# Performance work log

Measured on AMD Instinct MI355X. Metric: run time of the kernel, lower is better.

## Reference

```python
import jax, jax.numpy as jnp
import numpy as np
from jax import lax

D_MODEL = 512
D_STATE = 32
D_CONV = 4
D_INNER = 2 * D_MODEL
DT_RANK = (D_MODEL + 15) // 16  # 32
B_SZ, L = 8, 1024
EPS = 1e-12


def _mamba_params(key, pfx):
    ks = jax.random.split(key, 6)
    s = 0.02
    p = {}
    p[pfx + '_in_w'] = jax.random.normal(ks[0], (2 * D_INNER, D_MODEL)) * s
    p[pfx + '_conv_w'] = jax.random.normal(ks[1], (D_INNER, D_CONV)) * s
    p[pfx + '_conv_b'] = jnp.zeros((D_INNER,))
    p[pfx + '_xproj_w'] = jax.random.normal(ks[2], (DT_RANK + 2 * D_STATE, D_INNER)) * s
    p[pfx + '_dt_w'] = jax.random.normal(ks[3], (D_INNER, DT_RANK)) * s
    p[pfx + '_dt_b'] = jax.random.uniform(ks[4], (D_INNER,), minval=-4.0, maxval=-2.0)
    p[pfx + '_A_log'] = jnp.log(jnp.broadcast_to(jnp.arange(1, D_STATE + 1, dtype=jnp.float32), (D_INNER, D_STATE)))
    p[pfx + '_D'] = jnp.ones((D_INNER,))
    p[pfx + '_out_w'] = jax.random.normal(ks[5], (D_MODEL, D_INNER)) * s
    return p


def setup_inputs() -> dict:
    key = jax.random.key(0)
    ks = jax.random.split(key, 10)
    inp = {
        'hidden_states': jax.random.normal(ks[0], (B_SZ, L, D_MODEL)),
        'lengths': jax.random.randint(ks[1], (B_SZ,), 1, L + 1, dtype=jnp.int32),
    }
    inp.update(_mamba_params(ks[2], 'f'))
    inp.update(_mamba_params(ks[3], 'b'))
    s = 0.02
    inp['proj_w'] = jax.random.normal(ks[4], (1, 2)) * 0.5 + 0.5
    inp['proj_b'] = jnp.zeros((1,))
    inp['ln_g'] = jnp.ones((D_MODEL,))
    inp['ln_b'] = jnp.zeros((D_MODEL,))
    inp['ffn_w1'] = jax.random.normal(ks[5], (4 * D_MODEL, D_MODEL)) * s
    inp['ffn_b1'] = jnp.zeros((4 * D_MODEL,))
    inp['ffn_w2'] = jax.random.normal(ks[6], (D_MODEL, 4 * D_MODEL)) * s
    inp['ffn_b2'] = jnp.zeros((D_MODEL,))
    inp['ffn_ln_g'] = jnp.ones((D_MODEL,))
    inp['ffn_ln_b'] = jnp.zeros((D_MODEL,))
    return inp


def _layernorm(x, g, b):
    mu = jnp.mean(x, -1, keepdims=True)
    var = jnp.mean(jnp.square(x - mu), -1, keepdims=True)
    return (x - mu) * lax.rsqrt(var + EPS) * g + b


def _selective_scan(delta, Bm, Cm, u, A, D):
    # delta,u: (B,L,Di); Bm,Cm: (B,L,N); A: (Di,N); D: (Di,)
    def step(h, inp):
        d_t, B_t, C_t, u_t = inp
        dA = jnp.exp(d_t[..., None] * A)                 # (B,Di,N)
        h = dA * h + (d_t * u_t)[..., None] * B_t[:, None, :]
        y = jnp.einsum('bdn,bn->bd', h, C_t)
        return h, y
    h0 = jnp.zeros((u.shape[0], A.shape[0], A.shape[1]), u.dtype)
    xs = (delta.transpose(1, 0, 2), Bm.transpose(1, 0, 2),
          Cm.transpose(1, 0, 2), u.transpose(1, 0, 2))
    _, ys = lax.scan(step, h0, xs)
    return ys.transpose(1, 0, 2) + u * D


def _mamba(x, in_w, conv_w, conv_b, xproj_w, dt_w, dt_b, A_log, Dp, out_w):
    xz = jnp.einsum('bld,ed->ble', x, in_w)              # (B,L,2Di)
    x_in, z = jnp.split(xz, 2, axis=-1)
    # causal depthwise conv1d
    xc = jnp.pad(x_in.transpose(0, 2, 1), ((0, 0), (0, 0), (D_CONV - 1, 0)))
    xc = lax.conv_general_dilated(xc, conv_w[:, None, :], (1,), 'VALID',
                                  dimension_numbers=('NCH', 'OIH', 'NCH'),
                                  feature_group_count=D_INNER)
    xc = jax.nn.silu(xc + conv_b[None, :, None]).transpose(0, 2, 1)  # (B,L,Di)
    x_dbl = jnp.einsum('bld,ed->ble', xc, xproj_w)
    dt, Bm, Cm = jnp.split(x_dbl, [DT_RANK, DT_RANK + D_STATE], axis=-1)
    delta = jax.nn.softplus(jnp.einsum('blr,dr->bld', dt, dt_w) + dt_b)
    A = -jnp.exp(A_log)
    y = _selective_scan(delta, Bm, Cm, xc, A, Dp)
    y = y * jax.nn.silu(z)
    return jnp.einsum('bld,ed->ble', y, out_w)


def reference(hidden_states, lengths,
              f_in_w, f_conv_w, f_conv_b, f_xproj_w, f_dt_w, f_dt_b, f_A_log, f_D, f_out_w,
              b_in_w, b_conv_w, b_conv_b, b_xproj_w, b_dt_w, b_dt_b, b_A_log, b_D, b_out_w,
              proj_w, proj_b, ln_g, ln_b,
              ffn_w1, ffn_b1, ffn_w2, ffn_b2, ffn_ln_g, ffn_ln_b):
    x = hidden_states
    hf = _mamba(x, f_in_w, f_conv_w, f_conv_b, f_xproj_w, f_dt_w, f_dt_b, f_A_log, f_D, f_out_w)
    hb = _mamba(jnp.flip(x, 1), b_in_w, b_conv_w, b_conv_b, b_xproj_w, b_dt_w, b_dt_b, b_A_log, b_D, b_out_w)
    hb = jnp.flip(hb, 1)
    # Linear(2,1) over stacked [hf,hb] on last axis
    out = hf * proj_w[0, 0] + hb * proj_w[0, 1] + proj_b[0]
    out1 = _layernorm(out + x, ln_g, ln_b)  # dropout = identity (eval)
    h = jax.nn.gelu(jnp.einsum('bld,ed->ble', out1, ffn_w1) + ffn_b1, approximate=False)
    h = jnp.einsum('ble,de->bld', h, ffn_w2) + ffn_b2
    return _layernorm(h + out1, ffn_ln_g, ffn_ln_b)
```

## Files before the change

kernel.cpp:

```cpp
#include <hip/hip_runtime.h>
#include <hip/hip_bf16.h>
#include <hip/hip_fp16.h>
#include <math.h>

typedef __hip_bfloat16 bf16;
typedef __attribute__((ext_vector_type(8))) short bfrag;
typedef __attribute__((ext_vector_type(4))) float ffrag;
typedef __attribute__((ext_vector_type(4))) float f4;
typedef __attribute__((ext_vector_type(4))) short sh4;

#define BSZ    8
#define LSEQ   1024
#define DMODEL 512
#define DINNER 1024
#define DSTATE 32
#define DTRANK 32
#define MROWS  (BSZ * LSEQ)

__device__ __forceinline__ float bf2f(bf16 v) { return __bfloat162float(v); }
__device__ __forceinline__ float s2f(short s) {
    union { unsigned u; float f; } c; c.u = ((unsigned)(unsigned short)s) << 16; return c.f;
}
__device__ __forceinline__ short f2s(float v) {
    union { bf16 b; short s; } u; u.b = __float2bfloat16(v); return u.s;
}
__device__ __forceinline__ void stC(float* p, size_t i, float v) { p[i] = v; }
__device__ __forceinline__ void stC(bf16* p, size_t i, float v) { p[i] = __float2bfloat16(v); }
__device__ __forceinline__ float fsigmoid(float x) {
    return __builtin_amdgcn_rcpf(1.f + __expf(-x));
}
__device__ __forceinline__ float fexp2(float x) { return __builtin_amdgcn_exp2f(x); }

__device__ __forceinline__ float dload(const void* p, size_t i, int f) {
    if (f == 1) return ((const float*)p)[i];
    if (f == 2) return __half2float(((const __half*)p)[i]);
    if (f == 3) return (float)((const double*)p)[i];
    return bf2f(((const bf16*)p)[i]);
}

enum { ACT_NONE = 0, ACT_SOFTPLUS = 1, ACT_GELU = 2 };

__global__ void resolve_kernel(const void* a8, const void* d9, const void* d22,
                               const void* s0, const void* s1, int* flags)
{
    if (threadIdx.x != 0 || blockIdx.x != 0) return;
    const int cand[4] = {1, 0, 2, 3};
    int fw = -1;
    for (int ci = 0; ci < 4 && fw < 0; ++ci) {
        int f = cand[ci];
        bool ok = true;
        for (int k = 0; k < 48 && ok; ++k) {
            float e = logf((float)((k & 31) + 1));
            float v = dload(a8, k, f);
            ok = (v == v) && fabsf(v - e) <= 0.02f * e + 0.02f;
        }
        for (int k = 0; k < 8 && ok; ++k)
            ok = fabsf(dload(d9, k, f) - 1.f) <= 0.01f &&
                 fabsf(dload(d22, k, f) - 1.f) <= 0.01f;
        if (ok) fw = f;
    }
    int fx = -1, xs = -1;
    for (int si = 0; si < 2 && fx < 0; ++si) {
        const void* p = (si == 0) ? s0 : s1;
        for (int ci = 0; ci < 4 && fx < 0; ++ci) {
            int f = cand[ci];
            bool ok = true;
            float s = 0.f, s2 = 0.f;
            for (int k = 0; k < 256 && ok; ++k) {
                float v = dload(p, k, f);
                ok = (v == v) && fabsf(v) < 16.f;
                s += v; s2 += v * v;
            }
            if (ok) {
                float mu = s * (1.f / 256.f);
                float var = s2 * (1.f / 256.f) - mu * mu;
                if (var > 0.25f && var < 4.f) { fx = f; xs = si; }
            }
        }
    }
    flags[0] = (fw < 0) ? 1 : fw;
    flags[1] = (fx < 0) ? 1 : fx;
    flags[2] = (xs < 0) ? 0 : xs;
    flags[3] = (fw == 1 && fx == 1) ? 1 : 0;
}

__global__ __launch_bounds__(256) void cvt_x_kernel(const void* x0, const void* x1,
                                                    bf16* __restrict__ dst,
                                                    const int* __restrict__ flags)
{
    const void* x = flags[2] ? x1 : x0;
    const int fx = flags[1];
    int i = blockIdx.x * 256 + threadIdx.x;
    if (fx == 1) {
        f4 v = ((const f4*)x)[i];
        sh4 o;
#pragma unroll
        for (int j = 0; j < 4; ++j) o[j] = f2s(v[j]);
        ((sh4*)dst)[i] = o;
    } else {
#pragma unroll
        for (int j = 0; j < 4; ++j)
            dst[(size_t)i * 4 + j] = __float2bfloat16(dload(x, (size_t)i * 4 + j, fx));
    }
}

__global__ __launch_bounds__(256) void cvt3_kernel(
    const float* __restrict__ s0, bf16* __restrict__ d0, int n0,
    const float* __restrict__ s1, bf16* __restrict__ d1, int n1,
    const float* __restrict__ s2, bf16* __restrict__ d2, int n2)
{
    int i = blockIdx.x * 256 + threadIdx.x;
    const float* s; bf16* d; int off;
    if (i < n0) { s = s0; d = d0; off = i; }
    else if (i < n0 + n1) { s = s1; d = d1; off = i - n0; }
    else if (i < n0 + n1 + n2) { s = s2; d = d2; off = i - n0 - n1; }
    else return;
    f4 v = ((const f4*)s)[off];
    sh4 o;
#pragma unroll
    for (int j = 0; j < 4; ++j) o[j] = f2s(v[j]);
    ((sh4*)d)[off] = o;
}

__global__ __launch_bounds__(256) void transpose_kernel(
    const bf16* __restrict__ src, bf16* __restrict__ dst, int R, int D)
{
    __shared__ short t[64][72];
    const int r0 = blockIdx.x * 64, d0 = blockIdx.y * 64;
    const int tr = threadIdx.x >> 3;
    const int tc = (threadIdx.x & 7) * 8;
#pragma unroll
    for (int h = 0; h < 2; ++h) {
        int d = tr + h * 32;
        bfrag v = *(const bfrag*)&src[(size_t)(d0 + d) * R + r0 + tc];
#pragma unroll
        for (int j = 0; j < 8; ++j) t[tc + j][d] = v[j];
    }
    __syncthreads();
#pragma unroll
    for (int h = 0; h < 2; ++h) {
        int r = tr + h * 32;
        bfrag v = *(const bfrag*)&t[r][tc];
        *(bfrag*)&dst[(size_t)(r0 + r) * D + d0 + tc] = v;
    }
}

__global__ __launch_bounds__(256) void transpose_f32_kernel(
    const float* __restrict__ src, float* __restrict__ dst, int R)
{
    __shared__ float t[64][68];
    const int m0 = blockIdx.x * 64;
    const int tr = threadIdx.x >> 2;
    const int tc = (threadIdx.x & 3) * 16;
#pragma unroll
    for (int j = 0; j < 4; ++j) {
        f4 v = *(const f4*)&src[(size_t)tr * R + m0 + tc + j * 4];
#pragma unroll
        for (int e = 0; e < 4; ++e) t[tc + j * 4 + e][tr] = v[e];
    }
    __syncthreads();
#pragma unroll
    for (int j = 0; j < 4; ++j) {
        f4 v = *(const f4*)&t[tr][tc + j * 4];
        *(f4*)&dst[(size_t)(m0 + tr) * 64 + tc + j * 4] = v;
    }
}

__device__ __forceinline__ void glds16(const bf16* g, short* l)
{
    __builtin_amdgcn_global_load_lds(
        (const __attribute__((address_space(1))) void*)g,
        (__attribute__((address_space(3))) void*)l,
        16, 0, 0);
}

template <int FLIPB, int ACT, typename CT>
__global__ __launch_bounds__(256) void bgemm_kernel(
    const bf16* __restrict__ A, int lda,
    const bf16* __restrict__ B, int ldb,
    const float* __restrict__ bias,
    CT* __restrict__ C, int ldc, int K)
{
    __shared__ __align__(16) short As[128 * 32];
    __shared__ __align__(16) short Bs[128 * 32];
    const int tid = threadIdx.x;
    const int bm = blockIdx.y * 128, bn = blockIdx.x * 128;
    const int lane = tid & 63, w = tid >> 6;

    const int srow = lane >> 2;
    const int skc  = (lane & 3) << 3;
    const int arow0 = bm + w * 32 + srow;
    int brow0 = bn + w * 32 + srow;
    int brow1 = brow0 + 16;
    if (FLIPB) {
        brow0 = (brow0 & ~(LSEQ - 1)) + (LSEQ - 1 - (brow0 & (LSEQ - 1)));
        brow1 = (brow1 & ~(LSEQ - 1)) + (LSEQ - 1 - (brow1 & (LSEQ - 1)));
    }
    const bf16* ga0 = A + (size_t)arow0 * lda + skc;
    const bf16* ga1 = ga0 + (size_t)16 * lda;
    const bf16* gb0 = B + (size_t)brow0 * ldb + skc;
    const bf16* gb1 = B + (size_t)brow1 * ldb + skc;
    short* la0 = &As[(w * 32) * 32];
    short* la1 = &As[(w * 32 + 16) * 32];
    short* lb0 = &Bs[(w * 32) * 32];
    short* lb1 = &Bs[(w * 32 + 16) * 32];

    const int wm = (w & 1) << 6, wn = (w >> 1) << 6;
    const int lm = lane & 15, quad = lane >> 4;

    ffrag acc[4][4];
#pragma unroll
    for (int i = 0; i < 4; ++i)
#pragma unroll
        for (int j = 0; j < 4; ++j)
#pragma unroll
            for (int e = 0; e < 4; ++e) acc[i][j][e] = 0.f;

    for (int k0 = 0; k0 < K; k0 += 32) {
        glds16(ga0 + k0, la0);
        glds16(ga1 + k0, la1);
        glds16(gb0 + k0, lb0);
        glds16(gb1 + k0, lb1);
        __syncthreads();
        bfrag af[4], bfv[4];
#pragma unroll
        for (int ti = 0; ti < 4; ++ti)
            af[ti] = *(const bfrag*)&As[(wm + ti * 16 + lm) * 32 + quad * 8];
#pragma unroll
        for (int tj = 0; tj < 4; ++tj)
            bfv[tj] = *(const bfrag*)&Bs[(wn + tj * 16 + lm) * 32 + quad * 8];
#pragma unroll
        for (int ti = 0; ti < 4; ++ti)
#pragma unroll
            for (int tj = 0; tj < 4; ++tj)
                acc[ti][tj] = __builtin_amdgcn_mfma_f32_16x16x32_bf16(
                    af[ti], bfv[tj], acc[ti][tj], 0, 0, 0);
        __syncthreads();
    }

#pragma unroll
    for (int tj = 0; tj < 4; ++tj) {
        int col = bn + wn + tj * 16 + lm;
        float bcv = bias ? bias[col] : 0.f;
#pragma unroll
        for (int ti = 0; ti < 4; ++ti) {
#pragma unroll
            for (int r2 = 0; r2 < 4; ++r2) {
                int rowg = bm + wm + ti * 16 + quad * 4 + r2;
                float v = acc[ti][tj][r2] + bcv;
                if (ACT == ACT_GELU) v = 0.5f * v * (1.f + erff(v * 0.70710678118654752f));
                stC(C, (size_t)rowg * ldc + col, v);
            }
        }
    }
}

template <int ACT, typename CT>
__global__ __launch_bounds__(256) void bgemm64_kernel(
    const bf16* __restrict__ A, int lda,
    const bf16* __restrict__ B, int ldb,
    const float* __restrict__ bias,
    CT* __restrict__ C, int ldc, int M, int K)
{
    __shared__ __align__(16) short As[128 * 64];
    __shared__ __align__(16) short Bs[64 * 64];
    const int tid = threadIdx.x;
    const int bm = blockIdx.y * 128, bn = blockIdx.x * 64;
    const int lane = tid & 63, w = tid >> 6;

    const int lr = lane >> 3;
    const int sc = ((lane & 7) ^ lr) << 3;

    const bf16* ga[4];
#pragma unroll
    for (int a = 0; a < 4; ++a) {
        int ar = bm + w * 32 + a * 8 + lr;
        if (ar >= M) ar = M - 1;
        ga[a] = A + (size_t)ar * lda + sc;
    }
    const bf16* gb[2];
#pragma unroll
    for (int a = 0; a < 2; ++a) {
        int br = bn + w * 16 + a * 8 + lr;
        gb[a] = B + (size_t)br * ldb + sc;
    }
    short* la = &As[(w * 32) * 64];
    short* lb = &Bs[(w * 16) * 64];

    const int wm = (w & 1) << 6, wn = (w >> 1) << 5;
    const int lm = lane & 15, quad = lane >> 4;

    ffrag acc[4][2];
#pragma unroll
    for (int i = 0; i < 4; ++i)
#pragma unroll
        for (int j = 0; j < 2; ++j)
#pragma unroll
            for (int e = 0; e < 4; ++e) acc[i][j][e] = 0.f;

    for (int k0 = 0; k0 < K; k0 += 64) {
#pragma unroll
        for (int a = 0; a < 4; ++a) glds16(ga[a] + k0, la + a * 8 * 64);
#pragma unroll
        for (int a = 0; a < 2; ++a) glds16(gb[a] + k0, lb + a * 8 * 64);
        __syncthreads();
        bfrag af[2][4], bfv[2][2];
#pragma unroll
        for (int kk = 0; kk < 2; ++kk) {
#pragma unroll
            for (int ti = 0; ti < 4; ++ti) {
                int row = wm + ti * 16 + lm;
                int c = kk * 4 + quad;
                af[kk][ti] = *(const bfrag*)&As[row * 64 + ((c ^ (row & 7)) << 3)];
            }
#pragma unroll
            for (int tj = 0; tj < 2; ++tj) {
                int row = wn + tj * 16 + lm;
                int c = kk * 4 + quad;
                bfv[kk][tj] = *(const bfrag*)&Bs[row * 64 + ((c ^ (row & 7)) << 3)];
            }
        }
#pragma unroll
        for (int kk = 0; kk < 2; ++kk)
#pragma unroll
            for (int ti = 0; ti < 4; ++ti)
#pragma unroll
                for (int tj = 0; tj < 2; ++tj)
                    acc[ti][tj] = __builtin_amdgcn_mfma_f32_16x16x32_bf16(
                        af[kk][ti], bfv[kk][tj], acc[ti][tj], 0, 0, 0);
        __syncthreads();
    }

#pragma unroll
    for (int tj = 0; tj < 2; ++tj) {
        int col = bn + wn + tj * 16 + lm;
        float bcv = bias ? bias[col] : 0.f;
#pragma unroll
        for (int ti = 0; ti < 4; ++ti) {
#pragma unroll
            for (int r2 = 0; r2 < 4; ++r2) {
                int rowg = bm + wm + ti * 16 + quad * 4 + r2;
                if (rowg < M) {
                    float v = acc[ti][tj][r2] + bcv;
                    if (ACT == ACT_GELU) v = 0.5f * v * (1.f + erff(v * 0.70710678118654752f));
                    stC(C, (size_t)rowg * ldc + col, v);
                }
            }
        }
    }
}

__global__ __launch_bounds__(256) void dt_kernel(
    const float* __restrict__ xdT,
    const float* __restrict__ dt_w,
    const float* __restrict__ dt_b,
    bf16* __restrict__ delta_T)
{
    const int m = blockIdx.x * 256 + threadIdx.x;
    const int d0 = blockIdx.y * 64;
    float v[32];
#pragma unroll
    for (int r = 0; r < 32; ++r) v[r] = xdT[(size_t)r * MROWS + m];
    for (int d = d0; d < d0 + 64; ++d) {
        float acc = dt_b[d];
#pragma unroll
        for (int r = 0; r < 32; ++r) acc = fmaf(dt_w[d * 32 + r], v[r], acc);
        acc = (acc > 20.f) ? acc : log1pf(__expf(acc));
        delta_T[(size_t)d * MROWS + m] = __float2bfloat16(acc);
    }
}

__global__ __launch_bounds__(256) void conv_silu_kernel(
    const bf16* __restrict__ xin_T,
    const void* __restrict__ cw,
    const void* __restrict__ cb,
    bf16* __restrict__ u_T,
    const int* __restrict__ flags)
{
    const int fw = flags[0];
    int blk = blockIdx.x;
    int chunk = blk & 3;
    int db = blk >> 2;
    int b = db & 7;
    int d = db >> 3;
    int l = chunk * 256 + threadIdx.x;
    size_t base = (size_t)d * MROWS + b * LSEQ;
    float w0 = dload(cw, d * 4 + 0, fw), w1 = dload(cw, d * 4 + 1, fw);
    float w2 = dload(cw, d * 4 + 2, fw), w3 = dload(cw, d * 4 + 3, fw);
    float acc = dload(cb, d, fw);
    if (l >= 3) acc += bf2f(xin_T[base + l - 3]) * w0;
    if (l >= 2) acc += bf2f(xin_T[base + l - 2]) * w1;
    if (l >= 1) acc += bf2f(xin_T[base + l - 1]) * w2;
    acc += bf2f(xin_T[base + l]) * w3;
    u_T[base + l] = __float2bfloat16(acc * fsigmoid(acc));
}

#define SCH 8
struct ScanBuf { float dl[SCH], uv[SCH], Bv[SCH], Cv[SCH]; float zsc, usc; };

__device__ __forceinline__ void scan_load(ScanBuf& s,
    const bf16* __restrict__ dT, const bf16* __restrict__ uT,
    const bf16* __restrict__ zT, const float* __restrict__ xm,
    size_t lb, size_t mb, int n)
{
    bfrag dv = *(const bfrag*)&dT[lb];
    bfrag uv = *(const bfrag*)&uT[lb];
#pragma unroll
    for (int j = 0; j < SCH; ++j) { s.dl[j] = s2f(dv[j]); s.uv[j] = s2f(uv[j]); }
    s.zsc = bf2f(zT[lb + (n & 7)]);
    s.usc = bf2f(uT[lb + (n & 7)]);
#pragma unroll
    for (int j = 0; j < SCH; ++j) {
        s.Bv[j] = xm[(mb + j) * 64 + n];
        s.Cv[j] = xm[(mb + j) * 64 + 32 + n];
    }
}

__device__ __forceinline__ void scan_compute(const ScanBuf& s, float& h,
    float Ad2, float Dd, bf16* __restrict__ yT, size_t lb,
    bool b0, bool b1, bool b2, bool wr)
{
    float p[SCH];
#pragma unroll
    for (int j = 0; j < SCH; ++j) {
        float dlv = s.dl[j];
        h = fexp2(dlv * Ad2) * h + dlv * s.uv[j] * s.Bv[j];
        p[j] = h * s.Cv[j];
    }
    float q[4];
#pragma unroll
    for (int jj = 0; jj < 4; ++jj) {
        float keep = b0 ? p[2 * jj + 1] : p[2 * jj];
        float send = b0 ? p[2 * jj] : p[2 * jj + 1];
        q[jj] = keep + __shfl_xor(send, 1);
    }
    float r0 = (b1 ? q[1] : q[0]) + __shfl_xor(b1 ? q[0] : q[1], 2);
    float r1 = (b1 ? q[3] : q[2]) + __shfl_xor(b1 ? q[2] : q[3], 2);
    float t = (b2 ? r1 : r0) + __shfl_xor(b2 ? r0 : r1, 4);
    t += __shfl_xor(t, 8);
    t += __shfl_xor(t, 16);
    if (wr) {
        float y = t + s.usc * Dd;
        float g = s.zsc;
        y *= g * fsigmoid(g);
        yT[lb + (threadIdx.x & 7)] = __float2bfloat16(y);
    }
}

__global__ __launch_bounds__(256) void scan_kernel(
    const bf16* __restrict__ delta_T,
    bf16* __restrict__ u_T,
    const bf16* __restrict__ z_T,
    const float* __restrict__ xdbl_m,
    const void* __restrict__ A_log,
    const void* __restrict__ Dp,
    const int* __restrict__ flags)
{
    const int fw = flags[0];
    const int tid = threadIdx.x;
    const int n = tid & 31;
    const int dloc = tid >> 5;
    const int gd = blockIdx.x * 8 + dloc;
    const int b = gd >> 10;
    const int d = gd & (DINNER - 1);
    const bool b0 = n & 1, b1 = n & 2, b2 = n & 4;
    const bool wr = (n < 8);

    const float Ad2 = -__expf(dload(A_log, d * DSTATE + n, fw)) * 1.44269504088896341f;
    const float Dd = dload(Dp, d, fw);
    const size_t lbase = (size_t)d * MROWS + b * LSEQ;
    const size_t mbase = (size_t)b * LSEQ;
    float h = 0.f;

    ScanBuf bufA, bufB;
    scan_load(bufA, delta_T, u_T, z_T, xdbl_m, lbase, mbase, n);
    for (int c0 = 0; c0 < LSEQ / SCH; c0 += 2) {
        scan_load(bufB, delta_T, u_T, z_T, xdbl_m,
                  lbase + (size_t)(c0 + 1) * SCH, mbase + (size_t)(c0 + 1) * SCH, n);
        scan_compute(bufA, h, Ad2, Dd, u_T, lbase + (size_t)c0 * SCH, b0, b1, b2, wr);
        if (c0 + 2 < LSEQ / SCH)
            scan_load(bufA, delta_T, u_T, z_T, xdbl_m,
                      lbase + (size_t)(c0 + 2) * SCH, mbase + (size_t)(c0 + 2) * SCH, n);
        scan_compute(bufB, h, Ad2, Dd, u_T, lbase + (size_t)(c0 + 1) * SCH, b0, b1, b2, wr);
    }
}

__global__ __launch_bounds__(256) void combine_ln_kernel(
    const bf16* __restrict__ hf, const bf16* __restrict__ hb,
    const void* __restrict__ x0, const void* __restrict__ x1,
    const void* __restrict__ pw, const void* __restrict__ pb,
    const void* __restrict__ g, const void* __restrict__ be,
    bf16* __restrict__ out1,
    const int* __restrict__ flags)
{
    const int fw = flags[0];
    const int fx = flags[1];
    const void* x = flags[2] ? x1 : x0;
    int row = blockIdx.x;
    int b = row >> 10, l = row & (LSEQ - 1);
    int rrow = (b << 10) + (LSEQ - 1 - l);
    float pw0 = dload(pw, 0, fw), pw1 = dload(pw, 1, fw), pbv = dload(pb, 0, fw);
    __shared__ float red[2][4];
    float v[2], s = 0.f, s2 = 0.f;
#pragma unroll
    for (int i = 0; i < 2; ++i) {
        int c = threadIdx.x + i * 256;
        float val = bf2f(hf[(size_t)row * DMODEL + c]) * pw0
                  + bf2f(hb[(size_t)rrow * DMODEL + c]) * pw1
                  + pbv + dload(x, (size_t)row * DMODEL + c, fx);
        v[i] = val; s += val; s2 += val * val;
    }
    for (int m = 1; m < 64; m <<= 1) { s += __shfl_xor(s, m); s2 += __shfl_xor(s2, m); }
    int w = threadIdx.x >> 6;
    if ((threadIdx.x & 63) == 0) { red[0][w] = s; red[1][w] = s2; }
    __syncthreads();
    s = red[0][0] + red[0][1] + red[0][2] + red[0][3];
    s2 = red[1][0] + red[1][1] + red[1][2] + red[1][3];
    float mu = s * (1.f / DMODEL);
    float var = s2 * (1.f / DMODEL) - mu * mu;
    float r = rsqrtf(fmaxf(var, 0.f) + 1e-12f);
#pragma unroll
    for (int i = 0; i < 2; ++i) {
        int c = threadIdx.x + i * 256;
        float val = (v[i] - mu) * r * dload(g, c, fw) + dload(be, c, fw);
        out1[(size_t)row * DMODEL + c] = __float2bfloat16(val);
    }
}

__global__ __launch_bounds__(256) void final_ln_kernel(
    const float* __restrict__ out2, const bf16* __restrict__ out1,
    const void* __restrict__ g, const void* __restrict__ be,
    float* __restrict__ out,
    const int* __restrict__ flags)
{
    const int fw = flags[0];
    const int valid = flags[3];
    int row = blockIdx.x;
    __shared__ float red[2][4];
    float v[2], s = 0.f, s2 = 0.f;
#pragma unroll
    for (int i = 0; i < 2; ++i) {
        int c = threadIdx.x + i * 256;
        float val = out2[(size_t)row * DMODEL + c] + bf2f(out1[(size_t)row * DMODEL + c]);
        v[i] = val; s += val; s2 += val * val;
    }
    for (int m = 1; m < 64; m <<= 1) { s += __shfl_xor(s, m); s2 += __shfl_xor(s2, m); }
    int w = threadIdx.x >> 6;
    if ((threadIdx.x & 63) == 0) { red[0][w] = s; red[1][w] = s2; }
    __syncthreads();
    s = red[0][0] + red[0][1] + red[0][2] + red[0][3];
    s2 = red[1][0] + red[1][1] + red[1][2] + red[1][3];
    float mu = s * (1.f / DMODEL);
    float var = s2 * (1.f / DMODEL) - mu * mu;
    float r = rsqrtf(fmaxf(var, 0.f) + 1e-12f);
#pragma unroll
    for (int i = 0; i < 2; ++i) {
        int c = threadIdx.x + i * 256;
        float val = (v[i] - mu) * r * dload(g, c, fw) + dload(be, c, fw);
        out[(size_t)row * DMODEL + c] = valid ? val : 0.f;
    }
}

extern "C" void kernel_launch(void* const* d_in, const int* in_sizes, int n_in,
                              void* d_out, int out_size, void* d_ws, size_t ws_size,
                              hipStream_t stream)
{
    const void* x0 = d_in[0];
    const void* x1 = d_in[1];
    const void* proj_w   = d_in[20];
    const void* proj_b   = d_in[21];
    const void* ln_g     = d_in[22];
    const void* ln_b     = d_in[23];
    const float* ffn_w1  = (const float*)d_in[24];
    const float* ffn_b1  = (const float*)d_in[25];
    const float* ffn_w2  = (const float*)d_in[26];
    const float* ffn_b2  = (const float*)d_in[27];
    const void* ffn_ln_g = d_in[28];
    const void* ffn_ln_b = d_in[29];

    char* wsb = (char*)d_ws;
    char* ob  = (char*)d_out;
    bf16*  xin_T   = (bf16*)(wsb + 0);
    bf16*  z_T     = (bf16*)(wsb + (16u << 20));
    bf16*  uy_T    = (bf16*)(wsb + (32u << 20));
    bf16*  u_rm    = (bf16*)(wsb + 0);
    bf16*  delta_T = (bf16*)(wsb + 0);
    bf16*  y_rm    = (bf16*)(wsb + 0);
    float* xdT     = (float*)(wsb + (48u << 20));
    bf16*  in_w_bf = (bf16*)(wsb + (51u << 20));
    float* xdbl_m  = (float*)(wsb + (51u << 20));
    bf16*  xp_w_bf = (bf16*)(wsb + (53u << 20));
    bf16*  o_w_bf  = (bf16*)(wsb + (54u << 20));
    bf16*  hf      = (bf16*)d_out;
    bf16*  hb      = (bf16*)d_out + (size_t)MROWS * DMODEL;
    bf16*  xbf     = (bf16*)(ob + (8u << 20));
    bf16*  w1bf    = (bf16*)(ob + 0);
    bf16*  w2bf    = (bf16*)(ob + (2u << 20));
    bf16*  out1    = (bf16*)(wsb + 0);
    bf16*  ffn_h   = (bf16*)(wsb + (8u << 20));
    float* out2    = (float*)(wsb + (40u << 20));
    int*   flags   = (int*)(wsb + (56u << 20));

    dim3 blk(256);

    resolve_kernel<<<dim3(1), dim3(64), 0, stream>>>(
        d_in[8], d_in[9], d_in[22], x0, x1, flags);
    cvt_x_kernel<<<dim3(4096), blk, 0, stream>>>(x0, x1, xbf, flags);

    for (int dir = 0; dir < 2; ++dir) {
        int pb0 = 2 + dir * 9;
        const float* in_w    = (const float*)d_in[pb0 + 0];
        const void*  conv_w  = d_in[pb0 + 1];
        const void*  conv_b  = d_in[pb0 + 2];
        const float* xproj_w = (const float*)d_in[pb0 + 3];
        const float* dt_w    = (const float*)d_in[pb0 + 4];
        const float* dt_b    = (const float*)d_in[pb0 + 5];
        const void*  A_log   = d_in[pb0 + 6];
        const void*  Dp      = d_in[pb0 + 7];
        const float* out_w   = (const float*)d_in[pb0 + 8];
        bf16* hout = (dir == 0) ? hf : hb;

        cvt3_kernel<<<dim3(1632), blk, 0, stream>>>(
            in_w, in_w_bf, (2048 * 512) / 4,
            xproj_w, xp_w_bf, (96 * 1024) / 4,
            out_w, o_w_bf, (512 * 1024) / 4);

        if (dir == 0)
            bgemm_kernel<0, ACT_NONE, bf16><<<dim3(64, 16), blk, 0, stream>>>(
                in_w_bf, DMODEL, xbf, DMODEL, nullptr, xin_T, MROWS, DMODEL);
        else
            bgemm_kernel<1, ACT_NONE, bf16><<<dim3(64, 16), blk, 0, stream>>>(
                in_w_bf, DMODEL, xbf, DMODEL, nullptr, xin_T, MROWS, DMODEL);

        conv_silu_kernel<<<dim3(DINNER * BSZ * 4), blk, 0, stream>>>(
            xin_T, conv_w, conv_b, uy_T, flags);
        transpose_kernel<<<dim3(128, 16), blk, 0, stream>>>(uy_T, u_rm, MROWS, DINNER);
        bgemm64_kernel<ACT_NONE, float><<<dim3(128, 1), blk, 0, stream>>>(
            xp_w_bf, DINNER, u_rm, DINNER, nullptr, xdT, MROWS, 96, DINNER);
        transpose_f32_kernel<<<dim3(128), blk, 0, stream>>>(
            xdT + (size_t)32 * MROWS, xdbl_m, MROWS);
        dt_kernel<<<dim3(32, 16), blk, 0, stream>>>(xdT, dt_w, dt_b, delta_T);
        scan_kernel<<<dim3((BSZ * DINNER) / 8), blk, 0, stream>>>(
            delta_T, uy_T, z_T, xdbl_m, A_log, Dp, flags);
        transpose_kernel<<<dim3(128, 16), blk, 0, stream>>>(uy_T, y_rm, MROWS, DINNER);
        bgemm64_kernel<ACT_NONE, bf16><<<dim3(8, 64), blk, 0, stream>>>(
            y_rm, DINNER, o_w_bf, DINNER, nullptr, hout, DMODEL, MROWS, DINNER);
    }

    combine_ln_kernel<<<dim3(MROWS), blk, 0, stream>>>(
        hf, hb, x0, x1, proj_w, proj_b, ln_g, ln_b, out1, flags);
    cvt3_kernel<<<dim3(2048), blk, 0, stream>>>(
        ffn_w1, w1bf, (2048 * 512) / 4,
        ffn_w2, w2bf, (512 * 2048) / 4,
        nullptr, nullptr, 0);
    bgemm_kernel<0, ACT_GELU, bf16><<<dim3(16, 64), blk, 0, stream>>>(
        out1, DMODEL, w1bf, DMODEL, ffn_b1, ffn_h, 2048, DMODEL);
    bgemm64_kernel<ACT_NONE, float><<<dim3(8, 64), blk, 0, stream>>>(
        ffn_h, 2048, w2bf, 2048, ffn_b2, out2, DMODEL, MROWS, 2048);
    final_ln_kernel<<<dim3(MROWS), blk, 0, stream>>>(
        out2, out1, ffn_ln_g, ffn_ln_b, (float*)d_out, flags);
}
```

Before: 925.8 us.

## Double-buffer LDS tiles in bf16 GEMMs and parallelize dtype-resolve kernel across a wavefront

Both GEMM kernels now keep two LDS buffers and issue the global-to-LDS loads for the next K tile before computing on the current one, so a single barrier per iteration replaces the load-then-sync pattern. The intent is to overlap memory latency with MFMA work. Shared memory use doubles, which can lower occupancy. The single-thread dtype detection kernel is also spread across a wavefront, using ballots and shuffle reductions to cut its serial latency.

New measurement: 869.3 us. -6.1%, faster.

```diff
diff --git a/kernel.cpp b/kernel.cpp
--- a/kernel.cpp
+++ b/kernel.cpp
@@ -43,21 +43,23 @@
 __global__ void resolve_kernel(const void* a8, const void* d9, const void* d22,
                                const void* s0, const void* s1, int* flags)
 {
-    if (threadIdx.x != 0 || blockIdx.x != 0) return;
+    if (blockIdx.x != 0) return;
+    const int lane = threadIdx.x;
     const int cand[4] = {1, 0, 2, 3};
     int fw = -1;
     for (int ci = 0; ci < 4 && fw < 0; ++ci) {
         int f = cand[ci];
         bool ok = true;
-        for (int k = 0; k < 48 && ok; ++k) {
-            float e = logf((float)((k & 31) + 1));
-            float v = dload(a8, k, f);
+        if (lane < 48) {
+            float e = logf((float)((lane & 31) + 1));
+            float v = dload(a8, lane, f);
             ok = (v == v) && fabsf(v - e) <= 0.02f * e + 0.02f;
-        }
-        for (int k = 0; k < 8 && ok; ++k)
+        } else if (lane < 56) {
+            int k = lane - 48;
             ok = fabsf(dload(d9, k, f) - 1.f) <= 0.01f &&
                  fabsf(dload(d22, k, f) - 1.f) <= 0.01f;
-        if (ok) fw = f;
+        }
+        if (__all(ok)) fw = f;
     }
     int fx = -1, xs = -1;
     for (int si = 0; si < 2 && fx < 0; ++si) {
@@ -66,22 +68,28 @@
             int f = cand[ci];
             bool ok = true;
             float s = 0.f, s2 = 0.f;
-            for (int k = 0; k < 256 && ok; ++k) {
+            for (int k = lane; k < 256; k += 64) {
                 float v = dload(p, k, f);
-                ok = (v == v) && fabsf(v) < 16.f;
+                ok = ok && (v == v) && fabsf(v) < 16.f;
                 s += v; s2 += v * v;
             }
-            if (ok) {
+            int allok = __all(ok);
+            for (int m = 1; m < 64; m <<= 1) {
+                s += __shfl_xor(s, m); s2 += __shfl_xor(s2, m);
+            }
+            if (allok) {
                 float mu = s * (1.f / 256.f);
                 float var = s2 * (1.f / 256.f) - mu * mu;
                 if (var > 0.25f && var < 4.f) { fx = f; xs = si; }
             }
         }
     }
-    flags[0] = (fw < 0) ? 1 : fw;
-    flags[1] = (fx < 0) ? 1 : fx;
-    flags[2] = (xs < 0) ? 0 : xs;
-    flags[3] = (fw == 1 && fx == 1) ? 1 : 0;
+    if (lane == 0) {
+        flags[0] = (fw < 0) ? 1 : fw;
+        flags[1] = (fx < 0) ? 1 : fx;
+        flags[2] = (xs < 0) ? 0 : xs;
+        flags[3] = (fw == 1 && fx == 1) ? 1 : 0;
+    }
 }
 
 __global__ __launch_bounds__(256) void cvt_x_kernel(const void* x0, const void* x1,
@@ -181,8 +189,8 @@
     const float* __restrict__ bias,
     CT* __restrict__ C, int ldc, int K)
 {
-    __shared__ __align__(16) short As[128 * 32];
-    __shared__ __align__(16) short Bs[128 * 32];
+    __shared__ __align__(16) short As[2][128 * 32];
+    __shared__ __align__(16) short Bs[2][128 * 32];
     const int tid = threadIdx.x;
     const int bm = blockIdx.y * 128, bn = blockIdx.x * 128;
     const int lane = tid & 63, w = tid >> 6;
@@ -200,10 +208,7 @@
     const bf16* ga1 = ga0 + (size_t)16 * lda;
     const bf16* gb0 = B + (size_t)brow0 * ldb + skc;
     const bf16* gb1 = B + (size_t)brow1 * ldb + skc;
-    short* la0 = &As[(w * 32) * 32];
-    short* la1 = &As[(w * 32 + 16) * 32];
-    short* lb0 = &Bs[(w * 32) * 32];
-    short* lb1 = &Bs[(w * 32 + 16) * 32];
+    const int lA0 = (w * 32) * 32, lA1 = (w * 32 + 16) * 32;
 
     const int wm = (w & 1) << 6, wn = (w >> 1) << 6;
     const int lm = lane & 15, quad = lane >> 4;
@@ -216,19 +221,27 @@
 #pragma unroll
             for (int e = 0; e < 4; ++e) acc[i][j][e] = 0.f;
 
+    glds16(ga0, &As[0][lA0]);
+    glds16(ga1, &As[0][lA1]);
+    glds16(gb0, &Bs[0][lA0]);
+    glds16(gb1, &Bs[0][lA1]);
+    __syncthreads();
+
+    int cur = 0;
     for (int k0 = 0; k0 < K; k0 += 32) {
-        glds16(ga0 + k0, la0);
-        glds16(ga1 + k0, la1);
-        glds16(gb0 + k0, lb0);
-        glds16(gb1 + k0, lb1);
-        __syncthreads();
+        if (k0 + 32 < K) {
+            glds16(ga0 + k0 + 32, &As[cur ^ 1][lA0]);
+            glds16(ga1 + k0 + 32, &As[cur ^ 1][lA1]);
+            glds16(gb0 + k0 + 32, &Bs[cur ^ 1][lA0]);
+            glds16(gb1 + k0 + 32, &Bs[cur ^ 1][lA1]);
+        }
         bfrag af[4], bfv[4];
 #pragma unroll
         for (int ti = 0; ti < 4; ++ti)
-            af[ti] = *(const bfrag*)&As[(wm + ti * 16 + lm) * 32 + quad * 8];
+            af[ti] = *(const bfrag*)&As[cur][(wm + ti * 16 + lm) * 32 + quad * 8];
 #pragma unroll
         for (int tj = 0; tj < 4; ++tj)
-            bfv[tj] = *(const bfrag*)&Bs[(wn + tj * 16 + lm) * 32 + quad * 8];
+            bfv[tj] = *(const bfrag*)&Bs[cur][(wn + tj * 16 + lm) * 32 + quad * 8];
 #pragma unroll
         for (int ti = 0; ti < 4; ++ti)
 #pragma unroll
@@ -236,6 +249,7 @@
                 acc[ti][tj] = __builtin_amdgcn_mfma_f32_16x16x32_bf16(
                     af[ti], bfv[tj], acc[ti][tj], 0, 0, 0);
         __syncthreads();
+        cur ^= 1;
     }
 
 #pragma unroll
@@ -262,8 +276,8 @@
     const float* __restrict__ bias,
     CT* __restrict__ C, int ldc, int M, int K)
 {
-    __shared__ __align__(16) short As[128 * 64];
-    __shared__ __align__(16) short Bs[64 * 64];
+    __shared__ __align__(16) short As[2][128 * 64];
+    __shared__ __align__(16) short Bs[2][64 * 64];
     const int tid = threadIdx.x;
     const int bm = blockIdx.y * 128, bn = blockIdx.x * 64;
     const int lane = tid & 63, w = tid >> 6;
@@ -284,8 +298,7 @@
         int br = bn + w * 16 + a * 8 + lr;
         gb[a] = B + (size_t)br * ldb + sc;
     }
-    short* la = &As[(w * 32) * 64];
-    short* lb = &Bs[(w * 16) * 64];
+    const int lA = (w * 32) * 64, lB = (w * 16) * 64;
 
     const int wm = (w & 1) << 6, wn = (w >> 1) << 5;
     const int lm = lane & 15, quad = lane >> 4;
@@ -298,12 +311,20 @@
 #pragma unroll
             for (int e = 0; e < 4; ++e) acc[i][j][e] = 0.f;
 
+#pragma unroll
+    for (int a = 0; a < 4; ++a) glds16(ga[a], &As[0][lA + a * 8 * 64]);
+#pragma unroll
+    for (int a = 0; a < 2; ++a) glds16(gb[a], &Bs[0][lB + a * 8 * 64]);
+    __syncthreads();
+
+    int cur = 0;
     for (int k0 = 0; k0 < K; k0 += 64) {
-#pragma unroll
-        for (int a = 0; a < 4; ++a) glds16(ga[a] + k0, la + a * 8 * 64);
-#pragma unroll
-        for (int a = 0; a < 2; ++a) glds16(gb[a] + k0, lb + a * 8 * 64);
-        __syncthreads();
+        if (k0 + 64 < K) {
+#pragma unroll
+            for (int a = 0; a < 4; ++a) glds16(ga[a] + k0 + 64, &As[cur ^ 1][lA + a * 8 * 64]);
+#pragma unroll
+            for (int a = 0; a < 2; ++a) glds16(gb[a] + k0 + 64, &Bs[cur ^ 1][lB + a * 8 * 64]);
+        }
         bfrag af[2][4], bfv[2][2];
 #pragma unroll
         for (int kk = 0; kk < 2; ++kk) {
@@ -311,13 +332,13 @@
             for (int ti = 0; ti < 4; ++ti) {
                 int row = wm + ti * 16 + lm;
                 int c = kk * 4 + quad;
-                af[kk][ti] = *(const bfrag*)&As[row * 64 + ((c ^ (row & 7)) << 3)];
+                af[kk][ti] = *(const bfrag*)&As[cur][row * 64 + ((c ^ (row & 7)) << 3)];
             }
 #pragma unroll
             for (int tj = 0; tj < 2; ++tj) {
                 int row = wn + tj * 16 + lm;
                 int c = kk * 4 + quad;
-                bfv[kk][tj] = *(const bfrag*)&Bs[row * 64 + ((c ^ (row & 7)) << 3)];
+                bfv[kk][tj] = *(const bfrag*)&Bs[cur][row * 64 + ((c ^ (row & 7)) << 3)];
             }
         }
 #pragma unroll
@@ -329,6 +350,7 @@
                     acc[ti][tj] = __builtin_amdgcn_mfma_f32_16x16x32_bf16(
                         af[kk][ti], bfv[kk][tj], acc[ti][tj], 0, 0, 0);
         __syncthreads();
+        cur ^= 1;
     }
 
 #pragma unroll
```
